# Performance work log

Hardware: AMD Instinct MI355X
Metric: run time of the kernel (lower is better)

The kernel has to match this reference:

```python
import jax, jax.numpy as jnp
import numpy as np

VOCAB = 30522
EMBED = 768
NUM_CAT = 18
HIS = 50
CLICK_DIM = 100


def setup_inputs() -> dict:
    key = jax.random.key(0)
    ks = jax.random.split(key, 12)
    B, H, S = 64, HIS, 32
    encoding = jax.random.randint(ks[0], (B, H, S), 0, VOCAB)
    attention_mask = jnp.ones((B, H, S), dtype=bool)
    category_mask = jax.random.randint(ks[1], (B, NUM_CAT, H), 0, 2).astype(bool)
    inv = 1.0 / np.sqrt(EMBED)
    return {
        "encoding": encoding,
        "attention_mask": attention_mask,
        "category_mask": category_mask,
        "word_emb": jax.random.normal(ks[2], (VOCAB, EMBED), jnp.float32) * 0.02,
        "proj_w": jax.random.normal(ks[3], (EMBED, EMBED), jnp.float32) * inv,
        "proj_b": jnp.zeros((EMBED,), jnp.float32),
        "category_embedding": jax.random.normal(ks[4], (NUM_CAT, EMBED), jnp.float32) * 0.02,
        "w_news_attn": jax.random.normal(ks[5], (EMBED,), jnp.float32) * inv,
        "w_cat_attn": jax.random.normal(ks[6], (EMBED,), jnp.float32) * inv,
        "num_click_emb": jax.random.normal(ks[7], (HIS + 1, CLICK_DIM), jnp.float32) * 0.02,
        "click_w": jax.random.normal(ks[8], (CLICK_DIM,), jnp.float32) * (1.0 / np.sqrt(CLICK_DIM)),
        "click_b": jnp.zeros((), jnp.float32),
    }


def reference(encoding, attention_mask, category_mask, word_emb, proj_w, proj_b,
              category_embedding, w_news_attn, w_cat_attn, num_click_emb, click_w, click_b):
    # --- news_encoder stand-in: embedding lookup + masked mean pool + tanh(Linear) ---
    tok = word_emb[encoding]                                   # [B,H,S,E]
    m = attention_mask.astype(tok.dtype)[..., None]            # [B,H,S,1]
    pooled = (tok * m).sum(axis=2) / jnp.maximum(m.sum(axis=2), 1.0)  # [B,H,E]
    news_repr = jnp.tanh(pooled @ proj_w + proj_b)             # [B,H,E]

    # --- per-category masked softmax attention over history ---
    news_w = news_repr @ w_news_attn                           # [B,H]
    neg_inf = jnp.float32(-jnp.inf)
    scores = jnp.where(category_mask, news_w[:, None, :], neg_inf)  # [B,C,H]
    attn = jnp.nan_to_num(jax.nn.softmax(scores, axis=-1))     # nan rows (empty cats) -> 0
    category_interest = jnp.einsum('bch,bhe->bce', attn, news_repr)  # [B,C,E]
    category_repr = category_interest + category_embedding     # [B,C,E]

    # --- category-level attention with num-click scoring ---
    cat_w = category_repr @ w_cat_attn                          # [B,C]
    count = category_mask.sum(axis=-1).astype(jnp.int32)        # [B,C], <= HIS
    click_score = num_click_emb[count] @ click_w + click_b      # [B,C]
    final = cat_w + click_score
    final = jnp.where(count == 0, neg_inf, final)
    final = jax.nn.softmax(final, axis=-1)                      # [B,C]
    user_repr = jnp.einsum('bc,bce->be', final, category_repr)  # [B,E]
    return category_repr, user_repr
```

## Files before the change

### kernel.cpp

```cpp
#include <hip/hip_runtime.h>
#include <hip/hip_bf16.h>
#include <math.h>

#define VOCAB 30522
#define EMBED 768
#define NUM_CAT 18
#define HIS 50
#define SEQ 32
#define BATCH 64
#define CLICK_DIM 100

typedef short v8s __attribute__((ext_vector_type(8)));
typedef float v4f __attribute__((ext_vector_type(4)));
typedef unsigned short v8u __attribute__((ext_vector_type(8)));

#define OFF_POOLED 0
#define OFF_WT     4915200
#define OFF_NR     6094848
#define OFF_NEWSW  15925248
#define OFF_FLAG   16177664
#define OFF_WTAB   16252928
#define WS_NEED    63134720ull

__device__ __forceinline__ bool read_mask(const void* p, int i, int flag) {
    if (flag == 0) return ((const int*)p)[i] != 0;
    if (flag == 1) return ((const unsigned char*)p)[i] != 0;
    return ((const float*)p)[i] != 0.0f;
}

__device__ __forceinline__ float bf2f(unsigned short u) {
    union { unsigned int i; float f; } cv;
    cv.i = ((unsigned int)u) << 16;
    return cv.f;
}
__device__ __forceinline__ unsigned short f2bf(float f) {
    __hip_bfloat16 h = __float2bfloat16(f);
    return *(unsigned short*)&h;
}

#define CONV_BLOCKS 2048
__global__ __launch_bounds__(256) void kprep(
        const float* __restrict__ W, __hip_bfloat16* __restrict__ Wt,
        const unsigned int* __restrict__ cm, int* __restrict__ flag_out,
        const float* __restrict__ wemb, unsigned short* __restrict__ wtab,
        float* __restrict__ news_w) {
    int blk = blockIdx.x;
    if (blk < 576) {
        __shared__ float t[32][33];
        int tx = threadIdx.x & 31, ty = threadIdx.x >> 5;
        int k0 = (blk % 24) * 32, n0 = (blk / 24) * 32;
        #pragma unroll
        for (int i = 0; i < 4; ++i)
            t[ty + i * 8][tx] = W[(size_t)(k0 + ty + i * 8) * EMBED + n0 + tx];
        __syncthreads();
        #pragma unroll
        for (int i = 0; i < 4; ++i)
            Wt[(size_t)(n0 + ty + i * 8) * EMBED + k0 + tx] =
                __float2bfloat16(t[tx][ty + i * 8]);
    } else if (blk == 576) {
        __shared__ int word_gt1, byte_gt1;
        if (threadIdx.x == 0) { word_gt1 = 0; byte_gt1 = 0; }
        __syncthreads();
        int lw = 0, lb = 0;
        for (int i = threadIdx.x; i < 14400; i += 256) {
            unsigned int v = cm[i];
            if (v > 1u) lw = 1;
            if ((v & 0xFFu) > 1u || ((v >> 8) & 0xFFu) > 1u ||
                ((v >> 16) & 0xFFu) > 1u || ((v >> 24) & 0xFFu) > 1u) lb = 1;
        }
        if (lw) atomicOr(&word_gt1, 1);
        if (lb) atomicOr(&byte_gt1, 1);
        for (int i = threadIdx.x; i < BATCH * HIS; i += 256) news_w[i] = 0.f;
        __syncthreads();
        if (threadIdx.x == 0) {
            int f = 0;
            if (word_gt1) f = byte_gt1 ? 2 : 1;
            *flag_out = f;
        }
    } else {
        const int N4 = (VOCAB * EMBED) / 4;
        int gtid = (blk - 577) * 256 + threadIdx.x;
        const float4* src = (const float4*)wemb;
        ushort4* dst = (ushort4*)wtab;
        for (int i = gtid; i < N4; i += CONV_BLOCKS * 256) {
            float4 v = src[i];
            ushort4 o;
            o.x = f2bf(v.x); o.y = f2bf(v.y); o.z = f2bf(v.z); o.w = f2bf(v.w);
            dst[i] = o;
        }
    }
}

__global__ __launch_bounds__(192) void k1b_pool(
        const int* __restrict__ enc, const void* amask,
        const unsigned short* __restrict__ wtab, __hip_bfloat16* __restrict__ pooled,
        const int* __restrict__ flagp) {
    int tid = threadIdx.x, lane = tid & 63;
    int blk = blockIdx.x;
    int flag = *flagp;
    int bh0 = blk * 2, bh1 = blk * 2 + 1;
    bool mm = (lane < 32) ? read_mask(amask, bh0 * SEQ + lane, flag)
                          : read_mask(amask, bh1 * SEQ + (lane - 32), flag);
    unsigned long long bal = __ballot(mm);
    unsigned int mb0 = (unsigned int)(bal & 0xFFFFFFFFull);
    unsigned int mb1 = (unsigned int)(bal >> 32);
    int half = (tid >= 96) ? 1 : 0;
    int bh = half ? bh1 : bh0;
    unsigned int mb = half ? mb1 : mb0;
    float cnt = (float)__popc(mb);
    int slot = tid - half * 96;
    const int* e = enc + bh * SEQ;
    float a[8] = {};
    #pragma unroll
    for (int s0 = 0; s0 < SEQ; s0 += 8) {
        v8u v[8];
        #pragma unroll
        for (int j = 0; j < 8; ++j)
            v[j] = ((const v8u*)(wtab + (size_t)e[s0 + j] * EMBED))[slot];
        #pragma unroll
        for (int j = 0; j < 8; ++j) {
            float m = ((mb >> (s0 + j)) & 1u) ? 1.0f : 0.0f;
            #pragma unroll
            for (int k = 0; k < 8; ++k) a[k] += m * bf2f(v[j][k]);
        }
    }
    float d = 1.0f / fmaxf(cnt, 1.0f);
    v8u o;
    #pragma unroll
    for (int k = 0; k < 8; ++k) o[k] = f2bf(a[k] * d);
    *(v8u*)(((unsigned short*)pooled) + (size_t)bh * EMBED + slot * 8) = o;
}

__global__ __launch_bounds__(1024) void k0_detect(
        const unsigned int* __restrict__ cm, int* flag_out, float* __restrict__ news_w) {
    __shared__ int word_gt1, byte_gt1;
    if (threadIdx.x == 0) { word_gt1 = 0; byte_gt1 = 0; }
    __syncthreads();
    int lw = 0, lb = 0;
    for (int i = threadIdx.x; i < 14400; i += blockDim.x) {
        unsigned int v = cm[i];
        if (v > 1u) lw = 1;
        if ((v & 0xFFu) > 1u || ((v >> 8) & 0xFFu) > 1u ||
            ((v >> 16) & 0xFFu) > 1u || ((v >> 24) & 0xFFu) > 1u) lb = 1;
    }
    if (lw) atomicOr(&word_gt1, 1);
    if (lb) atomicOr(&byte_gt1, 1);
    for (int i = threadIdx.x; i < BATCH * HIS; i += blockDim.x) news_w[i] = 0.f;
    __syncthreads();
    if (threadIdx.x == 0) {
        int f = 0;
        if (word_gt1) f = byte_gt1 ? 2 : 1;
        *flag_out = f;
    }
}

__global__ __launch_bounds__(256) void k2a_wt(
        const float* __restrict__ W, __hip_bfloat16* __restrict__ Wt) {
    __shared__ float t[32][33];
    int tx = threadIdx.x & 31, ty = threadIdx.x >> 5;
    int k0 = blockIdx.x * 32, n0 = blockIdx.y * 32;
    #pragma unroll
    for (int i = 0; i < 4; ++i)
        t[ty + i * 8][tx] = W[(size_t)(k0 + ty + i * 8) * EMBED + n0 + tx];
    __syncthreads();
    #pragma unroll
    for (int i = 0; i < 4; ++i)
        Wt[(size_t)(n0 + ty + i * 8) * EMBED + k0 + tx] =
            __float2bfloat16(t[tx][ty + i * 8]);
}

__global__ __launch_bounds__(192) void k1_pool(
        const int* __restrict__ enc, const void* amask,
        const float* __restrict__ wemb, __hip_bfloat16* __restrict__ pooled,
        const int* __restrict__ flagp) {
    int wave = threadIdx.x >> 6, lane = threadIdx.x & 63;
    int bh = blockIdx.x;
    int flag = *flagp;
    const int* e = enc + bh * SEQ;
    bool m = (lane < SEQ) ? read_mask(amask, bh * SEQ + lane, flag) : false;
    unsigned long long mb = __ballot(m);
    float cnt = (float)__popcll(mb);
    int fslot = wave * 64 + lane;
    float ax = 0.f, ay = 0.f, az = 0.f, aw = 0.f;
    #pragma unroll
    for (int s0 = 0; s0 < SEQ; s0 += 8) {
        float4 v[8];
        #pragma unroll
        for (int j = 0; j < 8; ++j)
            v[j] = ((const float4*)(wemb + (size_t)e[s0 + j] * EMBED))[fslot];
        #pragma unroll
        for (int j = 0; j < 8; ++j) {
            float mmv = ((mb >> (s0 + j)) & 1ull) ? 1.0f : 0.0f;
            ax += mmv * v[j].x; ay += mmv * v[j].y;
            az += mmv * v[j].z; aw += mmv * v[j].w;
        }
    }
    float d = 1.0f / fmaxf(cnt, 1.0f);
    ushort4 pk;
    pk.x = f2bf(ax * d); pk.y = f2bf(ay * d);
    pk.z = f2bf(az * d); pk.w = f2bf(aw * d);
    *(ushort4*)((unsigned short*)pooled + (size_t)bh * EMBED + fslot * 4) = pk;
}

#define BM 64
#define BN 128
#define GBK 64
#define LDP 72
__global__ __launch_bounds__(256) void k2_mfma(
        const __hip_bfloat16* __restrict__ A,
        const __hip_bfloat16* __restrict__ Bt,
        const float* __restrict__ bias,
        const float* __restrict__ wna,
        float* __restrict__ C,
        float* __restrict__ news_w) {
    __shared__ short As[BM * LDP];
    __shared__ short Bs[BN * LDP];
    int tid = threadIdx.x;
    int wave = tid >> 6, lane = tid & 63;
    int l15 = lane & 15, l4 = lane >> 4;
    int wr = wave >> 1, wc = wave & 1;
    int row0 = blockIdx.x * BM;
    int col0 = blockIdx.y * BN;
    v4f acc[2][4] = {};

    int ra[2], ca[2], rb[4], cb[4];
    #pragma unroll
    for (int it = 0; it < 2; ++it) {
        int chunk = tid + it * 256;
        ra[it] = chunk >> 3; ca[it] = chunk & 7;
    }
    #pragma unroll
    for (int it = 0; it < 4; ++it) {
        int chunk = tid + it * 256;
        rb[it] = chunk >> 3; cb[it] = chunk & 7;
    }

    v8s pa[2], pb[4];
    #pragma unroll
    for (int it = 0; it < 2; ++it)
        pa[it] = *(const v8s*)(A  + (size_t)(row0 + ra[it]) * EMBED + ca[it] * 8);
    #pragma unroll
    for (int it = 0; it < 4; ++it)
        pb[it] = *(const v8s*)(Bt + (size_t)(col0 + rb[it]) * EMBED + cb[it] * 8);

    for (int s = 0; s < EMBED / GBK; ++s) {
        #pragma unroll
        for (int it = 0; it < 2; ++it)
            *(v8s*)&As[ra[it] * LDP + ca[it] * 8] = pa[it];
        #pragma unroll
        for (int it = 0; it < 4; ++it)
            *(v8s*)&Bs[rb[it] * LDP + cb[it] * 8] = pb[it];
        __syncthreads();
        if (s < EMBED / GBK - 1) {
            int k0 = (s + 1) * GBK;
            #pragma unroll
            for (int it = 0; it < 2; ++it)
                pa[it] = *(const v8s*)(A  + (size_t)(row0 + ra[it]) * EMBED + k0 + ca[it] * 8);
            #pragma unroll
            for (int it = 0; it < 4; ++it)
                pb[it] = *(const v8s*)(Bt + (size_t)(col0 + rb[it]) * EMBED + k0 + cb[it] * 8);
        }
        #pragma unroll
        for (int kk = 0; kk < 2; ++kk) {
            v8s af[2], bf_[4];
            #pragma unroll
            for (int mi = 0; mi < 2; ++mi)
                af[mi] = *(const v8s*)&As[(wr * 32 + mi * 16 + l15) * LDP + kk * 32 + l4 * 8];
            #pragma unroll
            for (int ni = 0; ni < 4; ++ni)
                bf_[ni] = *(const v8s*)&Bs[(wc * 64 + ni * 16 + l15) * LDP + kk * 32 + l4 * 8];
            #pragma unroll
            for (int mi = 0; mi < 2; ++mi)
                #pragma unroll
                for (int ni = 0; ni < 4; ++ni)
                    acc[mi][ni] = __builtin_amdgcn_mfma_f32_16x16x32_bf16(
                        af[mi], bf_[ni], acc[mi][ni], 0, 0, 0);
        }
        __syncthreads();
    }
    float bcol[4], wcol[4];
    #pragma unroll
    for (int ni = 0; ni < 4; ++ni) {
        int col = col0 + wc * 64 + ni * 16 + l15;
        bcol[ni] = bias[col]; wcol[ni] = wna[col];
    }
    #pragma unroll
    for (int mi = 0; mi < 2; ++mi) {
        #pragma unroll
        for (int r = 0; r < 4; ++r) {
            int row = row0 + wr * 32 + mi * 16 + l4 * 4 + r;
            float pr = 0.f;
            #pragma unroll
            for (int ni = 0; ni < 4; ++ni) {
                int col = col0 + wc * 64 + ni * 16 + l15;
                float tv = tanhf(acc[mi][ni][r] + bcol[ni]);
                C[(size_t)row * EMBED + col] = tv;
                pr += tv * wcol[ni];
            }
            pr += __shfl_xor(pr, 1); pr += __shfl_xor(pr, 2);
            pr += __shfl_xor(pr, 4); pr += __shfl_xor(pr, 8);
            if (l15 == 0) atomicAdd(&news_w[row], pr);
        }
    }
}

__global__ __launch_bounds__(768) void k4_fused(
        const void* cmask, const float* __restrict__ nr,
        const float* __restrict__ news_w, const float* __restrict__ cat_emb,
        const float* __restrict__ w_cat, const float* __restrict__ click_emb,
        const float* __restrict__ click_w, const float* __restrict__ click_b,
        float* __restrict__ out_cat, float* __restrict__ user,
        const int* __restrict__ flagp) {
    int b = blockIdx.x, tid = threadIdx.x;
    int wave = tid >> 6, lane = tid & 63;
    int flag = *flagp;
    __shared__ float plds[HIS][20];
    __shared__ float redbuf[NUM_CAT][12];
    __shared__ float clicks[NUM_CAT];
    __shared__ int   cnts[NUM_CAT];
    __shared__ float logit[NUM_CAT];

    for (int c = wave; c < NUM_CAT; c += 12) {
        bool m = false; float v = -INFINITY;
        if (lane < HIS) {
            m = read_mask(cmask, (b * NUM_CAT + c) * HIS + lane, flag);
            if (m) v = news_w[b * HIS + lane];
        }
        unsigned long long bal = __ballot(m);
        int cnt = __popcll(bal);
        float maxv = v;
        #pragma unroll
        for (int off = 32; off; off >>= 1) maxv = fmaxf(maxv, __shfl_xor(maxv, off));
        float e = (v == -INFINITY) ? 0.f : expf(v - maxv);
        float sum = e;
        #pragma unroll
        for (int off = 32; off; off >>= 1) sum += __shfl_xor(sum, off);
        if (lane < HIS)
            plds[lane][c] = (cnt == 0 || v == -INFINITY) ? 0.f : e / sum;
        float cs = 0.f;
        if (lane < HIS) {
            const float* ce = click_emb + (size_t)cnt * CLICK_DIM;
            cs = ce[lane] * click_w[lane] + ce[lane + HIS] * click_w[lane + HIS];
        }
        #pragma unroll
        for (int off = 32; off; off >>= 1) cs += __shfl_down(cs, off);
        if (lane == 0) { cnts[c] = cnt; clicks[c] = cs + click_b[0]; }
    }
    __syncthreads();

    int col = tid;
    const float* nrb = nr + (size_t)b * HIS * EMBED;
    float acc[NUM_CAT];
    #pragma unroll
    for (int c = 0; c < NUM_CAT; ++c) acc[c] = 0.f;
    #pragma unroll 5
    for (int h = 0; h < HIS; ++h) {
        float v = nrb[h * EMBED + col];
        #pragma unroll
        for (int c = 0; c < NUM_CAT; ++c) acc[c] += plds[h][c] * v;
    }
    float part[NUM_CAT];
    float wv = w_cat[col];
    float* ocb = out_cat + (size_t)b * NUM_CAT * EMBED;
    #pragma unroll
    for (int c = 0; c < NUM_CAT; ++c) {
        float o = acc[c] + cat_emb[c * EMBED + col];
        acc[c] = o;
        ocb[c * EMBED + col] = o;
        part[c] = o * wv;
    }
    #pragma unroll
    for (int c = 0; c < NUM_CAT; ++c) {
        float s = part[c];
        #pragma unroll
        for (int off = 32; off; off >>= 1) s += __shfl_down(s, off);
        if (lane == 0) redbuf[c][wave] = s;
    }
    __syncthreads();
    if (tid < NUM_CAT) {
        float s = 0.f;
        #pragma unroll
        for (int w = 0; w < 12; ++w) s += redbuf[tid][w];
        logit[tid] = (cnts[tid] == 0) ? -INFINITY : (s + clicks[tid]);
    }
    __syncthreads();

    float maxv = -INFINITY;
    #pragma unroll
    for (int c = 0; c < NUM_CAT; ++c) maxv = fmaxf(maxv, logit[c]);
    float sum = 0.f;
    #pragma unroll
    for (int c = 0; c < NUM_CAT; ++c)
        sum += (logit[c] == -INFINITY) ? 0.f : expf(logit[c] - maxv);
    float u = 0.f;
    #pragma unroll
    for (int c = 0; c < NUM_CAT; ++c) {
        float w = (logit[c] == -INFINITY) ? 0.f : expf(logit[c] - maxv) / sum;
        u += w * acc[c];
    }
    user[(size_t)b * EMBED + col] = u;
}

extern "C" void kernel_launch(void* const* d_in, const int* in_sizes, int n_in,
                              void* d_out, int out_size, void* d_ws, size_t ws_size,
                              hipStream_t stream) {
    const int*   enc    = (const int*)d_in[0];
    const void*  amask  = d_in[1];
    const void*  cmask  = d_in[2];
    const float* wemb   = (const float*)d_in[3];
    const float* projw  = (const float*)d_in[4];
    const float* projb  = (const float*)d_in[5];
    const float* catemb = (const float*)d_in[6];
    const float* wna    = (const float*)d_in[7];
    const float* wca    = (const float*)d_in[8];
    const float* clemb  = (const float*)d_in[9];
    const float* clw    = (const float*)d_in[10];
    const float* clb    = (const float*)d_in[11];

    unsigned char* wsb = (unsigned char*)d_ws;
    __hip_bfloat16* pooled = (__hip_bfloat16*)(wsb + OFF_POOLED);
    __hip_bfloat16* Wt     = (__hip_bfloat16*)(wsb + OFF_WT);
    float* nr     = (float*)(wsb + OFF_NR);
    float* news_w = (float*)(wsb + OFF_NEWSW);
    int*   flag   = (int*)(wsb + OFF_FLAG);
    unsigned short* wtab = (unsigned short*)(wsb + OFF_WTAB);

    float* out_cat = (float*)d_out;
    float* user    = (float*)d_out + BATCH * NUM_CAT * EMBED;

    if (ws_size >= WS_NEED) {
        kprep<<<577 + CONV_BLOCKS, 256, 0, stream>>>(
            projw, Wt, (const unsigned int*)cmask, flag, wemb, wtab, news_w);
        k1b_pool<<<1600, 192, 0, stream>>>(enc, amask, wtab, pooled, flag);
    } else {
        k0_detect<<<1, 1024, 0, stream>>>((const unsigned int*)cmask, flag, news_w);
        dim3 gt(24, 24);
        k2a_wt<<<gt, 256, 0, stream>>>(projw, Wt);
        k1_pool<<<3200, 192, 0, stream>>>(enc, amask, wemb, pooled, flag);
    }
    dim3 g2(50, 6);
    k2_mfma<<<g2, 256, 0, stream>>>(pooled, Wt, projb, wna, nr, news_w);
    k4_fused<<<BATCH, 768, 0, stream>>>(cmask, nr, news_w, catemb, wca,
                                        clemb, clw, clb, out_cat, user, flag);
}
```

Measured before the change: 88.94 us.

## Store news_repr in bf16, shrink GEMM tile, prefetch pool gathers, widen conversion

```diff
diff --git a/kernel.cpp b/kernel.cpp
--- a/kernel.cpp
+++ b/kernel.cpp
@@ -78,14 +78,15 @@
             *flag_out = f;
         }
     } else {
-        const int N4 = (VOCAB * EMBED) / 4;
+        const int N8 = (VOCAB * EMBED) / 8;
         int gtid = (blk - 577) * 256 + threadIdx.x;
         const float4* src = (const float4*)wemb;
-        ushort4* dst = (ushort4*)wtab;
-        for (int i = gtid; i < N4; i += CONV_BLOCKS * 256) {
-            float4 v = src[i];
-            ushort4 o;
-            o.x = f2bf(v.x); o.y = f2bf(v.y); o.z = f2bf(v.z); o.w = f2bf(v.w);
+        v8u* dst = (v8u*)wtab;
+        for (int i = gtid; i < N8; i += CONV_BLOCKS * 256) {
+            float4 a = src[2 * i], b = src[2 * i + 1];
+            v8u o;
+            o[0] = f2bf(a.x); o[1] = f2bf(a.y); o[2] = f2bf(a.z); o[3] = f2bf(a.w);
+            o[4] = f2bf(b.x); o[5] = f2bf(b.y); o[6] = f2bf(b.z); o[7] = f2bf(b.w);
             dst[i] = o;
         }
     }
@@ -111,18 +112,25 @@
     int slot = tid - half * 96;
     const int* e = enc + bh * SEQ;
     float a[8] = {};
+    v8u v[8], w[8];
+    #pragma unroll
+    for (int j = 0; j < 8; ++j)
+        v[j] = ((const v8u*)(wtab + (size_t)e[j] * EMBED))[slot];
     #pragma unroll
     for (int s0 = 0; s0 < SEQ; s0 += 8) {
-        v8u v[8];
-        #pragma unroll
-        for (int j = 0; j < 8; ++j)
-            v[j] = ((const v8u*)(wtab + (size_t)e[s0 + j] * EMBED))[slot];
+        if (s0 + 8 < SEQ) {
+            #pragma unroll
+            for (int j = 0; j < 8; ++j)
+                w[j] = ((const v8u*)(wtab + (size_t)e[s0 + 8 + j] * EMBED))[slot];
+        }
         #pragma unroll
         for (int j = 0; j < 8; ++j) {
             float m = ((mb >> (s0 + j)) & 1u) ? 1.0f : 0.0f;
             #pragma unroll
             for (int k = 0; k < 8; ++k) a[k] += m * bf2f(v[j][k]);
         }
+        #pragma unroll
+        for (int j = 0; j < 8; ++j) v[j] = w[j];
     }
     float d = 1.0f / fmaxf(cnt, 1.0f);
     v8u o;
@@ -203,7 +211,7 @@
 }
 
 #define BM 64
-#define BN 128
+#define BN 64
 #define GBK 64
 #define LDP 72
 __global__ __launch_bounds__(256) void k2_mfma(
@@ -211,7 +219,7 @@
         const __hip_bfloat16* __restrict__ Bt,
         const float* __restrict__ bias,
         const float* __restrict__ wna,
-        float* __restrict__ C,
+        unsigned short* __restrict__ C,
         float* __restrict__ news_w) {
     __shared__ short As[BM * LDP];
     __shared__ short Bs[BN * LDP];
@@ -221,67 +229,59 @@
     int wr = wave >> 1, wc = wave & 1;
     int row0 = blockIdx.x * BM;
     int col0 = blockIdx.y * BN;
-    v4f acc[2][4] = {};
-
-    int ra[2], ca[2], rb[4], cb[4];
+    v4f acc[2][2] = {};
+
+    int ra[2], ca[2];
     #pragma unroll
     for (int it = 0; it < 2; ++it) {
         int chunk = tid + it * 256;
         ra[it] = chunk >> 3; ca[it] = chunk & 7;
     }
-    #pragma unroll
-    for (int it = 0; it < 4; ++it) {
-        int chunk = tid + it * 256;
-        rb[it] = chunk >> 3; cb[it] = chunk & 7;
-    }
-
-    v8s pa[2], pb[4];
-    #pragma unroll
-    for (int it = 0; it < 2; ++it)
+
+    v8s pa[2], pb[2];
+    #pragma unroll
+    for (int it = 0; it < 2; ++it) {
         pa[it] = *(const v8s*)(A  + (size_t)(row0 + ra[it]) * EMBED + ca[it] * 8);
-    #pragma unroll
-    for (int it = 0; it < 4; ++it)
-        pb[it] = *(const v8s*)(Bt + (size_t)(col0 + rb[it]) * EMBED + cb[it] * 8);
+        pb[it] = *(const v8s*)(Bt + (size_t)(col0 + ra[it]) * EMBED + ca[it] * 8);
+    }
 
     for (int s = 0; s < EMBED / GBK; ++s) {
         #pragma unroll
-        for (int it = 0; it < 2; ++it)
+        for (int it = 0; it < 2; ++it) {
             *(v8s*)&As[ra[it] * LDP + ca[it] * 8] = pa[it];
-        #pragma unroll
-        for (int it = 0; it < 4; ++it)
-            *(v8s*)&Bs[rb[it] * LDP + cb[it] * 8] = pb[it];
+            *(v8s*)&Bs[ra[it] * LDP + ca[it] * 8] = pb[it];
+        }
         __syncthreads();
         if (s < EMBED / GBK - 1) {
             int k0 = (s + 1) * GBK;
             #pragma unroll
-            for (int it = 0; it < 2; ++it)
+            for (int it = 0; it < 2; ++it) {
                 pa[it] = *(const v8s*)(A  + (size_t)(row0 + ra[it]) * EMBED + k0 + ca[it] * 8);
-            #pragma unroll
-            for (int it = 0; it < 4; ++it)
-                pb[it] = *(const v8s*)(Bt + (size_t)(col0 + rb[it]) * EMBED + k0 + cb[it] * 8);
+                pb[it] = *(const v8s*)(Bt + (size_t)(col0 + ra[it]) * EMBED + k0 + ca[it] * 8);
+            }
         }
         #pragma unroll
         for (int kk = 0; kk < 2; ++kk) {
-            v8s af[2], bf_[4];
+            v8s af[2], bf_[2];
             #pragma unroll
             for (int mi = 0; mi < 2; ++mi)
                 af[mi] = *(const v8s*)&As[(wr * 32 + mi * 16 + l15) * LDP + kk * 32 + l4 * 8];
             #pragma unroll
-            for (int ni = 0; ni < 4; ++ni)
-                bf_[ni] = *(const v8s*)&Bs[(wc * 64 + ni * 16 + l15) * LDP + kk * 32 + l4 * 8];
+            for (int ni = 0; ni < 2; ++ni)
+                bf_[ni] = *(const v8s*)&Bs[(wc * 32 + ni * 16 + l15) * LDP + kk * 32 + l4 * 8];
             #pragma unroll
             for (int mi = 0; mi < 2; ++mi)
                 #pragma unroll
-                for (int ni = 0; ni < 4; ++ni)
+                for (int ni = 0; ni < 2; ++ni)
                     acc[mi][ni] = __builtin_amdgcn_mfma_f32_16x16x32_bf16(
                         af[mi], bf_[ni], acc[mi][ni], 0, 0, 0);
         }
         __syncthreads();
     }
-    float bcol[4], wcol[4];
-    #pragma unroll
-    for (int ni = 0; ni < 4; ++ni) {
-        int col = col0 + wc * 64 + ni * 16 + l15;
+    float bcol[2], wcol[2];
+    #pragma unroll
+    for (int ni = 0; ni < 2; ++ni) {
+        int col = col0 + wc * 32 + ni * 16 + l15;
         bcol[ni] = bias[col]; wcol[ni] = wna[col];
     }
     #pragma unroll
@@ -291,10 +291,10 @@
             int row = row0 + wr * 32 + mi * 16 + l4 * 4 + r;
             float pr = 0.f;
             #pragma unroll
-            for (int ni = 0; ni < 4; ++ni) {
-                int col = col0 + wc * 64 + ni * 16 + l15;
+            for (int ni = 0; ni < 2; ++ni) {
+                int col = col0 + wc * 32 + ni * 16 + l15;
                 float tv = tanhf(acc[mi][ni][r] + bcol[ni]);
-                C[(size_t)row * EMBED + col] = tv;
+                C[(size_t)row * EMBED + col] = f2bf(tv);
                 pr += tv * wcol[ni];
             }
             pr += __shfl_xor(pr, 1); pr += __shfl_xor(pr, 2);
@@ -305,7 +305,7 @@
 }
 
 __global__ __launch_bounds__(768) void k4_fused(
-        const void* cmask, const float* __restrict__ nr,
+        const void* cmask, const unsigned short* __restrict__ nr,
         const float* __restrict__ news_w, const float* __restrict__ cat_emb,
         const float* __restrict__ w_cat, const float* __restrict__ click_emb,
         const float* __restrict__ click_w, const float* __restrict__ click_b,
@@ -349,13 +349,13 @@
     __syncthreads();
 
     int col = tid;
-    const float* nrb = nr + (size_t)b * HIS * EMBED;
+    const unsigned short* nrb = nr + (size_t)b * HIS * EMBED;
     float acc[NUM_CAT];
     #pragma unroll
     for (int c = 0; c < NUM_CAT; ++c) acc[c] = 0.f;
     #pragma unroll 5
     for (int h = 0; h < HIS; ++h) {
-        float v = nrb[h * EMBED + col];
+        float v = bf2f(nrb[h * EMBED + col]);
         #pragma unroll
         for (int c = 0; c < NUM_CAT; ++c) acc[c] += plds[h][c] * v;
     }
@@ -420,7 +420,7 @@
     unsigned char* wsb = (unsigned char*)d_ws;
     __hip_bfloat16* pooled = (__hip_bfloat16*)(wsb + OFF_POOLED);
     __hip_bfloat16* Wt     = (__hip_bfloat16*)(wsb + OFF_WT);
-    float* nr     = (float*)(wsb + OFF_NR);
+    unsigned short* nr     = (unsigned short*)(wsb + OFF_NR);
     float* news_w = (float*)(wsb + OFF_NEWSW);
     int*   flag   = (int*)(wsb + OFF_FLAG);
     unsigned short* wtab = (unsigned short*)(wsb + OFF_WTAB);
@@ -438,7 +438,7 @@
         k2a_wt<<<gt, 256, 0, stream>>>(projw, Wt);
         k1_pool<<<3200, 192, 0, stream>>>(enc, amask, wemb, pooled, flag);
     }
-    dim3 g2(50, 6);
+    dim3 g2(50, 12);
     k2_mfma<<<g2, 256, 0, stream>>>(pooled, Wt, projb, wna, nr, news_w);
     k4_fused<<<BATCH, 768, 0, stream>>>(cmask, nr, news_w, catemb, wca,
                                         clemb, clw, clb, out_cat, user, flag);
```

Measured after the change: 87.28 us. No clear change (-1.9%).
